# Kernel optimization log

Hardware: AMD Instinct MI355X
Metric: run time of the kernel (lower is better)

The kernel has to match this reference:

```python
import jax, jax.numpy as jnp
import numpy as np

B, TQ, TS, E, D = 8, 100, 100, 512, 512

def setup_inputs() -> dict:
    key = jax.random.key(0)
    k1, k2, k3, k4, k5 = jax.random.split(key, 5)
    src_reps = jax.random.normal(k1, (B, TQ, TS, E), dtype=jnp.float32)
    tgt_reps = jax.random.normal(k2, (B, TQ, TS, E), dtype=jnp.float32)
    mask = jnp.ones((B, TQ, TS), dtype=jnp.float32)
    # attn_1: Linear(2E -> D) with bias; attn_2: Linear(D -> 1) no bias
    W1 = jax.random.normal(k3, (2 * E, D), dtype=jnp.float32) / np.sqrt(2 * E)
    b1 = jax.random.normal(k4, (D,), dtype=jnp.float32) * 0.01
    w2 = jax.random.normal(k5, (D,), dtype=jnp.float32) / np.sqrt(D)
    return {"src_reps": src_reps, "tgt_reps": tgt_reps, "mask": mask,
            "W1": W1, "b1": b1, "w2": w2}

def reference(src_reps, tgt_reps, mask, W1, b1, w2):
    # cat over feature dim: [B,TQ,TS,2E]
    cat_reps = jnp.concatenate([src_reps, tgt_reps], axis=-1)
    # two small linears + tanh -> scores [B,TQ,TS]
    h = jnp.tanh(jnp.einsum('bqse,ed->bqsd', cat_reps, W1) + b1)
    attn_scores = jnp.einsum('bqsd,d->bqs', h, w2)
    attn_scores = mask * attn_scores  # multiplicative mask (as in source)
    attn_weights = jax.nn.softmax(attn_scores, axis=2)
    # weighted sum over src dim -> [B,TQ,E]
    attn_out = jnp.einsum('bqs,bqse->bqe', attn_weights, src_reps)
    return (attn_out, attn_weights)
```

## Files before the change

kernel.cpp:

```cpp
#include <hip/hip_runtime.h>
#include <hip/hip_bf16.h>

#define B_   8
#define TQ_  100
#define TS_  100
#define E_   512
#define D_   512
#define K_   1024
#define M_   (B_*TQ_*TS_)

#define MT   64
#define BK   64
#define NTHREADS 512

typedef __attribute__((ext_vector_type(4))) float f32x4;
typedef __attribute__((ext_vector_type(8))) short bf16x8;

__device__ __forceinline__ short f2bf(float f) {
  __hip_bfloat16 h = __float2bfloat16(f);
  return *reinterpret_cast<short*>(&h);
}

__device__ __forceinline__ float fast_tanh(float x) {
  float e = __expf(2.0f * x);
  return 1.0f - 2.0f / (e + 1.0f);
}

__global__ void prep_w1(const float* __restrict__ W1, short* __restrict__ W1t) {
  int idx = blockIdx.x * 256 + threadIdx.x;
  int k = idx >> 9;
  int n = idx & (D_ - 1);
  W1t[(size_t)n * K_ + k] = f2bf(W1[idx]);
}

__launch_bounds__(NTHREADS, 4)
__global__ void scores_kernel(const float* __restrict__ src,
                              const float* __restrict__ tgt,
                              const short* __restrict__ W1t,
                              const float* __restrict__ b1,
                              const float* __restrict__ w2,
                              float* __restrict__ scores) {
  __shared__ __align__(16) char Alds[MT * 128];
  __shared__ __align__(16) char Blds[D_ * 128];
  __shared__ float s_sc[MT];

  const int tid  = threadIdx.x;
  const int wave = tid >> 6;
  const int lane = tid & 63;
  const int lr   = lane & 15;
  const int lg   = lane >> 4;
  const int m0   = blockIdx.x * MT;

  f32x4 acc[4][4];
  #pragma unroll
  for (int i = 0; i < 4; i++)
    #pragma unroll
    for (int j = 0; j < 4; j++)
      acc[i][j] = (f32x4){0.f, 0.f, 0.f, 0.f};

  const int ar = tid >> 3;
  const int ac = (tid & 7) * 8;

  for (int k0 = 0; k0 < K_; k0 += BK) {
    {
      const float* Ap = ((k0 < E_) ? src : tgt)
                        + (size_t)(m0 + ar) * E_ + (k0 & (E_ - 1)) + ac;
      f32x4 v0 = *reinterpret_cast<const f32x4*>(Ap);
      f32x4 v1 = *reinterpret_cast<const f32x4*>(Ap + 4);
      bf16x8 w;
      w[0] = f2bf(v0[0]); w[1] = f2bf(v0[1]); w[2] = f2bf(v0[2]); w[3] = f2bf(v0[3]);
      w[4] = f2bf(v1[0]); w[5] = f2bf(v1[1]); w[6] = f2bf(v1[2]); w[7] = f2bf(v1[3]);
      *reinterpret_cast<bf16x8*>(Alds + ar * 128 + ((ac * 2) ^ ((ar & 7) << 4))) = w;
    }
    #pragma unroll
    for (int i = 0; i < 8; i++) {
      int n = ar + i * 64;
      bf16x8 v = *reinterpret_cast<const bf16x8*>(W1t + (size_t)n * K_ + k0 + ac);
      *reinterpret_cast<bf16x8*>(Blds + n * 128 + ((ac * 2) ^ ((n & 7) << 4))) = v;
    }
    __syncthreads();

    #pragma unroll
    for (int kk = 0; kk < 2; kk++) {
      const int kb = kk * 64 + lg * 16;
      bf16x8 a[4], b[4];
      #pragma unroll
      for (int mi = 0; mi < 4; mi++) {
        int row = mi * 16 + lr;
        a[mi] = *reinterpret_cast<const bf16x8*>(
                    Alds + row * 128 + (kb ^ ((row & 7) << 4)));
      }
      #pragma unroll
      for (int ni = 0; ni < 4; ni++) {
        int n = wave * 64 + ni * 16 + lr;
        b[ni] = *reinterpret_cast<const bf16x8*>(
                    Blds + n * 128 + (kb ^ ((n & 7) << 4)));
      }
      #pragma unroll
      for (int mi = 0; mi < 4; mi++)
        #pragma unroll
        for (int ni = 0; ni < 4; ni++)
          acc[mi][ni] = __builtin_amdgcn_mfma_f32_16x16x32_bf16(
                            a[mi], b[ni], acc[mi][ni], 0, 0, 0);
    }
    __syncthreads();
  }

  if (tid < MT) s_sc[tid] = 0.0f;
  __syncthreads();

  float b1v[4], w2v[4];
  #pragma unroll
  for (int ni = 0; ni < 4; ni++) {
    int n = wave * 64 + ni * 16 + lr;
    b1v[ni] = b1[n];
    w2v[ni] = w2[n];
  }
  #pragma unroll
  for (int mi = 0; mi < 4; mi++) {
    #pragma unroll
    for (int r = 0; r < 4; r++) {
      float p = 0.0f;
      #pragma unroll
      for (int ni = 0; ni < 4; ni++)
        p += fast_tanh(acc[mi][ni][r] + b1v[ni]) * w2v[ni];
      p += __shfl_xor(p, 1);
      p += __shfl_xor(p, 2);
      p += __shfl_xor(p, 4);
      p += __shfl_xor(p, 8);
      if (lr == 0) atomicAdd(&s_sc[mi * 16 + lg * 4 + r], p);
    }
  }
  __syncthreads();
  if (tid < MT) scores[m0 + tid] = s_sc[tid];
}

__global__ void softmax_wsum(const float* __restrict__ src,
                             const float* __restrict__ mask,
                             const float* __restrict__ scores,
                             float* __restrict__ out) {
  const int row = blockIdx.x;
  const int tid = threadIdx.x;
  __shared__ float s_e[TS_];

  float v = 0.0f;
  if (tid < TS_) {
    v = scores[row * TS_ + tid] * mask[row * TS_ + tid];
    s_e[tid] = v;
  }
  __syncthreads();
  float mx = -3.0e38f;
  for (int s = 0; s < TS_; s++) mx = fmaxf(mx, s_e[s]);
  __syncthreads();
  if (tid < TS_) s_e[tid] = __expf(v - mx);
  __syncthreads();
  float sum = 0.0f;
  for (int s = 0; s < TS_; s++) sum += s_e[s];
  const float inv = 1.0f / sum;

  float* out_attn = out;
  float* out_w    = out + (size_t)B_ * TQ_ * E_;
  if (tid < TS_) out_w[row * TS_ + tid] = s_e[tid] * inv;

  const float* sp = src + (size_t)row * TS_ * E_ + tid;
  float acc = 0.0f;
  #pragma unroll 4
  for (int s = 0; s < TS_; s++) acc = fmaf(s_e[s], sp[(size_t)s * E_], acc);
  out_attn[row * E_ + tid] = acc * inv;
}

extern "C" void kernel_launch(void* const* d_in, const int* in_sizes, int n_in,
                              void* d_out, int out_size, void* d_ws, size_t ws_size,
                              hipStream_t stream) {
  const float* src  = (const float*)d_in[0];
  const float* tgt  = (const float*)d_in[1];
  const float* mask = (const float*)d_in[2];
  const float* W1   = (const float*)d_in[3];
  const float* b1   = (const float*)d_in[4];
  const float* w2   = (const float*)d_in[5];

  short* W1t    = (short*)d_ws;
  float* scores = (float*)((char*)d_ws + (size_t)D_ * K_ * 2);

  float* out = (float*)d_out;

  hipLaunchKernelGGL(prep_w1, dim3((K_ * D_) / 256), dim3(256), 0, stream, W1, W1t);
  hipLaunchKernelGGL(scores_kernel, dim3(M_ / MT), dim3(NTHREADS), 0, stream,
                     src, tgt, W1t, b1, w2, scores);
  hipLaunchKernelGGL(softmax_wsum, dim3(B_ * TQ_), dim3(512), 0, stream,
                     src, mask, scores, out);
}
```

Before: 161.3 us.

## Fuse score GEMM with softmax and weighted sum per query row

Merges the score GEMM and the softmax/weighted-sum kernels into one kernel, with one block per (b,q) row of 100 source positions, padded to 112. The bf16 copy of the src tile is kept in LDS so the weighted sum can reuse it, and the tgt half is double-buffered while the src half is staged. W1 is pre-packed into an MFMA-fragment layout and read directly from global/L2 instead of through LDS. This removes the scores round trip and one launch. In exchange it wastes 12 padded rows per block, runs fewer blocks at higher LDS use, and re-reads src in fp32 for the final sum.

Measured after the change: 206.3 us. +27.9%, slower.

```diff
diff --git a/kernel.cpp b/kernel.cpp
--- a/kernel.cpp
+++ b/kernel.cpp
@@ -1,16 +1,13 @@
 #include <hip/hip_runtime.h>
 #include <hip/hip_bf16.h>
 
-#define B_   8
 #define TQ_  100
 #define TS_  100
 #define E_   512
 #define D_   512
 #define K_   1024
-#define M_   (B_*TQ_*TS_)
-
-#define MT   64
-#define BK   64
+#define NBQ  800
+#define MR   112
 #define NTHREADS 512
 
 typedef __attribute__((ext_vector_type(4))) float f32x4;
@@ -26,88 +23,115 @@
   return 1.0f - 2.0f / (e + 1.0f);
 }
 
-__global__ void prep_w1(const float* __restrict__ W1, short* __restrict__ W1t) {
+__global__ void prep_w1(const float* __restrict__ W1, short* __restrict__ Bpk) {
   int idx = blockIdx.x * 256 + threadIdx.x;
   int k = idx >> 9;
   int n = idx & (D_ - 1);
-  W1t[(size_t)n * K_ + k] = f2bf(W1[idx]);
+  int kc = k >> 5, lg = (k >> 3) & 3, w = k & 7;
+  int nt = n >> 4, lr = n & 15;
+  Bpk[(((size_t)(nt * 32 + kc)) << 9) + (size_t)((lg * 16 + lr) << 3) + w] = f2bf(W1[idx]);
 }
 
-__launch_bounds__(NTHREADS, 4)
-__global__ void scores_kernel(const float* __restrict__ src,
-                              const float* __restrict__ tgt,
-                              const short* __restrict__ W1t,
-                              const float* __restrict__ b1,
-                              const float* __restrict__ w2,
-                              float* __restrict__ scores) {
-  __shared__ __align__(16) char Alds[MT * 128];
-  __shared__ __align__(16) char Blds[D_ * 128];
-  __shared__ float s_sc[MT];
+__launch_bounds__(NTHREADS, 2)
+__global__ void fused_kernel(const float* __restrict__ src,
+                             const float* __restrict__ tgt,
+                             const float* __restrict__ mask,
+                             const short* __restrict__ Bpk,
+                             const float* __restrict__ b1,
+                             const float* __restrict__ w2,
+                             float* __restrict__ out) {
+  __shared__ __align__(16) char As[MR * 1024];
+  __shared__ __align__(16) char At[2][MR * 128];
+  __shared__ float s_sc[MR];
+  __shared__ float s_e[TS_];
 
   const int tid  = threadIdx.x;
   const int wave = tid >> 6;
   const int lane = tid & 63;
   const int lr   = lane & 15;
   const int lg   = lane >> 4;
-  const int m0   = blockIdx.x * MT;
+  const int bq   = blockIdx.x;
+  const int nt0  = wave * 4;
 
-  f32x4 acc[4][4];
+  f32x4 acc[7][4];
   #pragma unroll
-  for (int i = 0; i < 4; i++)
+  for (int i = 0; i < 7; i++)
     #pragma unroll
     for (int j = 0; j < 4; j++)
       acc[i][j] = (f32x4){0.f, 0.f, 0.f, 0.f};
 
-  const int ar = tid >> 3;
-  const int ac = (tid & 7) * 8;
+  const int srow = tid >> 2;
+  const int ssub = tid & 3;
+  const bool stg = (srow < TS_);
+  const int ssw  = (srow & 7) << 4;
+  const float* srcg = src + ((size_t)bq * TS_) * E_;
+  const float* tgtg = tgt + ((size_t)bq * TS_) * E_;
 
-  for (int k0 = 0; k0 < K_; k0 += BK) {
-    {
-      const float* Ap = ((k0 < E_) ? src : tgt)
-                        + (size_t)(m0 + ar) * E_ + (k0 & (E_ - 1)) + ac;
-      f32x4 v0 = *reinterpret_cast<const f32x4*>(Ap);
-      f32x4 v1 = *reinterpret_cast<const f32x4*>(Ap + 4);
-      bf16x8 w;
-      w[0] = f2bf(v0[0]); w[1] = f2bf(v0[1]); w[2] = f2bf(v0[2]); w[3] = f2bf(v0[3]);
-      w[4] = f2bf(v1[0]); w[5] = f2bf(v1[1]); w[6] = f2bf(v1[2]); w[7] = f2bf(v1[3]);
-      *reinterpret_cast<bf16x8*>(Alds + ar * 128 + ((ac * 2) ^ ((ar & 7) << 4))) = w;
+  if (tid < MR) s_sc[tid] = 0.0f;
+
+  #define LOADQ(P, KF)                                                         \
+    { const float* p_ = (P) + (size_t)srow * E_ + (KF);                        \
+      q0 = *(const f32x4*)(p_);      q1 = *(const f32x4*)(p_ + 4);             \
+      q2 = *(const f32x4*)(p_ + 8);  q3 = *(const f32x4*)(p_ + 12); }
+
+  #define WRITEQ(BASE, RSTR, BOFF)                                             \
+    { bf16x8 w0, w1;                                                           \
+      w0[0]=f2bf(q0[0]); w0[1]=f2bf(q0[1]); w0[2]=f2bf(q0[2]); w0[3]=f2bf(q0[3]); \
+      w0[4]=f2bf(q1[0]); w0[5]=f2bf(q1[1]); w0[6]=f2bf(q1[2]); w0[7]=f2bf(q1[3]); \
+      w1[0]=f2bf(q2[0]); w1[1]=f2bf(q2[1]); w1[2]=f2bf(q2[2]); w1[3]=f2bf(q2[3]); \
+      w1[4]=f2bf(q3[0]); w1[5]=f2bf(q3[1]); w1[6]=f2bf(q3[2]); w1[7]=f2bf(q3[3]); \
+      *(bf16x8*)((BASE) + (size_t)srow * (RSTR) + (((BOFF)      ) ^ ssw)) = w0; \
+      *(bf16x8*)((BASE) + (size_t)srow * (RSTR) + (((BOFF) + 16) ^ ssw)) = w1; }
+
+  #define COMPUTE_KK(ABASE, RSTR, BYOFF, KC)                                   \
+    { bf16x8 b[4], a[7];                                                       \
+      _Pragma("unroll")                                                        \
+      for (int j = 0; j < 4; j++)                                              \
+        b[j] = *(const bf16x8*)(Bpk + (((size_t)((nt0 + j) * 32 + (KC))) << 9) \
+                                + (size_t)lane * 8);                           \
+      _Pragma("unroll")                                                        \
+      for (int mi = 0; mi < 7; mi++) {                                         \
+        int row = mi * 16 + lr;                                                \
+        a[mi] = *(const bf16x8*)((ABASE) + (size_t)row * (RSTR) +              \
+                    (((BYOFF) + lg * 16) ^ ((row & 7) << 4)));                 \
+      }                                                                        \
+      __builtin_amdgcn_s_setprio(1);                                           \
+      _Pragma("unroll")                                                        \
+      for (int mi = 0; mi < 7; mi++)                                           \
+        _Pragma("unroll")                                                      \
+        for (int ni = 0; ni < 4; ni++)                                         \
+          acc[mi][ni] = __builtin_amdgcn_mfma_f32_16x16x32_bf16(               \
+              a[mi], b[ni], acc[mi][ni], 0, 0, 0);                             \
+      __builtin_amdgcn_s_setprio(0); }
+
+  {
+    f32x4 q0, q1, q2, q3;
+    if (stg) { LOADQ(tgtg, ssub * 16); WRITEQ(At[0], 128, ssub * 32); }
+  }
+  __syncthreads();
+
+  for (int c = 0; c < 8; ++c) {
+    f32x4 q0, q1, q2, q3, p0, p1, p2, p3;
+    if (stg) {
+      if (c < 7) { LOADQ(tgtg, (c + 1) * 64 + ssub * 16); }
+      { const float* p_ = srcg + (size_t)srow * E_ + c * 64 + ssub * 16;
+        p0 = *(const f32x4*)(p_);      p1 = *(const f32x4*)(p_ + 4);
+        p2 = *(const f32x4*)(p_ + 8);  p3 = *(const f32x4*)(p_ + 12); }
     }
-    #pragma unroll
-    for (int i = 0; i < 8; i++) {
-      int n = ar + i * 64;
-      bf16x8 v = *reinterpret_cast<const bf16x8*>(W1t + (size_t)n * K_ + k0 + ac);
-      *reinterpret_cast<bf16x8*>(Blds + n * 128 + ((ac * 2) ^ ((n & 7) << 4))) = v;
-    }
-    __syncthreads();
-
-    #pragma unroll
-    for (int kk = 0; kk < 2; kk++) {
-      const int kb = kk * 64 + lg * 16;
-      bf16x8 a[4], b[4];
-      #pragma unroll
-      for (int mi = 0; mi < 4; mi++) {
-        int row = mi * 16 + lr;
-        a[mi] = *reinterpret_cast<const bf16x8*>(
-                    Alds + row * 128 + (kb ^ ((row & 7) << 4)));
-      }
-      #pragma unroll
-      for (int ni = 0; ni < 4; ni++) {
-        int n = wave * 64 + ni * 16 + lr;
-        b[ni] = *reinterpret_cast<const bf16x8*>(
-                    Blds + n * 128 + (kb ^ ((n & 7) << 4)));
-      }
-      #pragma unroll
-      for (int mi = 0; mi < 4; mi++)
-        #pragma unroll
-        for (int ni = 0; ni < 4; ni++)
-          acc[mi][ni] = __builtin_amdgcn_mfma_f32_16x16x32_bf16(
-                            a[mi], b[ni], acc[mi][ni], 0, 0, 0);
+    COMPUTE_KK(At[c & 1], 128,  0, 16 + 2 * c);
+    COMPUTE_KK(At[c & 1], 128, 64, 17 + 2 * c);
+    if (stg) {
+      if (c < 7) WRITEQ(At[(c + 1) & 1], 128, ssub * 32);
+      q0 = p0; q1 = p1; q2 = p2; q3 = p3;
+      WRITEQ(As, 1024, c * 128 + ssub * 32);
     }
     __syncthreads();
   }
 
-  if (tid < MT) s_sc[tid] = 0.0f;
-  __syncthreads();
+  for (int c = 0; c < 8; ++c) {
+    COMPUTE_KK(As, 1024, c * 128,      2 * c);
+    COMPUTE_KK(As, 1024, c * 128 + 64, 2 * c + 1);
+  }
 
   float b1v[4], w2v[4];
   #pragma unroll
@@ -117,7 +141,7 @@
     w2v[ni] = w2[n];
   }
   #pragma unroll
-  for (int mi = 0; mi < 4; mi++) {
+  for (int mi = 0; mi < 7; mi++) {
     #pragma unroll
     for (int r = 0; r < 4; r++) {
       float p = 0.0f;
@@ -132,41 +156,27 @@
     }
   }
   __syncthreads();
-  if (tid < MT) scores[m0 + tid] = s_sc[tid];
-}
 
-__global__ void softmax_wsum(const float* __restrict__ src,
-                             const float* __restrict__ mask,
-                             const float* __restrict__ scores,
-                             float* __restrict__ out) {
-  const int row = blockIdx.x;
-  const int tid = threadIdx.x;
-  __shared__ float s_e[TS_];
-
-  float v = 0.0f;
-  if (tid < TS_) {
-    v = scores[row * TS_ + tid] * mask[row * TS_ + tid];
-    s_e[tid] = v;
-  }
+  if (tid < TS_) s_e[tid] = s_sc[tid] * mask[(size_t)bq * TS_ + tid];
   __syncthreads();
   float mx = -3.0e38f;
   for (int s = 0; s < TS_; s++) mx = fmaxf(mx, s_e[s]);
   __syncthreads();
-  if (tid < TS_) s_e[tid] = __expf(v - mx);
+  if (tid < TS_) s_sc[tid] = __expf(s_e[tid] - mx);
   __syncthreads();
   float sum = 0.0f;
-  for (int s = 0; s < TS_; s++) sum += s_e[s];
+  for (int s = 0; s < TS_; s++) sum += s_sc[s];
   const float inv = 1.0f / sum;
 
   float* out_attn = out;
-  float* out_w    = out + (size_t)B_ * TQ_ * E_;
-  if (tid < TS_) out_w[row * TS_ + tid] = s_e[tid] * inv;
+  float* out_w    = out + (size_t)NBQ * E_;
+  if (tid < TS_) out_w[(size_t)bq * TS_ + tid] = s_sc[tid] * inv;
 
-  const float* sp = src + (size_t)row * TS_ * E_ + tid;
-  float acc = 0.0f;
+  const float* sp = srcg + tid;
+  float a2 = 0.0f;
   #pragma unroll 4
-  for (int s = 0; s < TS_; s++) acc = fmaf(s_e[s], sp[(size_t)s * E_], acc);
-  out_attn[row * E_ + tid] = acc * inv;
+  for (int s = 0; s < TS_; s++) a2 = fmaf(s_sc[s], sp[(size_t)s * E_], a2);
+  out_attn[(size_t)bq * E_ + tid] = a2 * inv;
 }
 
 extern "C" void kernel_launch(void* const* d_in, const int* in_sizes, int n_in,
@@ -179,14 +189,10 @@
   const float* b1   = (const float*)d_in[4];
   const float* w2   = (const float*)d_in[5];
 
-  short* W1t    = (short*)d_ws;
-  float* scores = (float*)((char*)d_ws + (size_t)D_ * K_ * 2);
-
+  short* Bpk = (short*)d_ws;
   float* out = (float*)d_out;
 
-  hipLaunchKernelGGL(prep_w1, dim3((K_ * D_) / 256), dim3(256), 0, stream, W1, W1t);
-  hipLaunchKernelGGL(scores_kernel, dim3(M_ / MT), dim3(NTHREADS), 0, stream,
-                     src, tgt, W1t, b1, w2, scores);
-  hipLaunchKernelGGL(softmax_wsum, dim3(B_ * TQ_), dim3(512), 0, stream,
-                     src, mask, scores, out);
+  hipLaunchKernelGGL(prep_w1, dim3((K_ * D_) / 256), dim3(256), 0, stream, W1, Bpk);
+  hipLaunchKernelGGL(fused_kernel, dim3(NBQ), dim3(NTHREADS), 0, stream,
+                     src, tgt, mask, Bpk, b1, w2, out);
 }
```
